# Optimization experiments

Measured on AMD Instinct MI355X. Metric: run time of the kernel, lower is better.

## Reference

```python
import jax, jax.numpy as jnp
import numpy as np

D_MODEL = 1024
NUM_HEADS = 16
MAX_SEQ_LEN = 2048
THETA = 10000.0
D_K = D_MODEL // NUM_HEADS


def setup_inputs() -> dict:
    key = jax.random.key(0)
    ks = jax.random.split(key, 5)
    x = jax.random.normal(ks[0], (2, 2048, D_MODEL), dtype=jnp.float32)
    token_positions = jnp.arange(2048, dtype=jnp.int32)
    s = 1.0 / np.sqrt(D_MODEL)
    w_q = jax.random.normal(ks[1], (D_MODEL, D_MODEL), dtype=jnp.float32) * s
    w_k = jax.random.normal(ks[2], (D_MODEL, D_MODEL), dtype=jnp.float32) * s
    w_v = jax.random.normal(ks[3], (D_MODEL, D_MODEL), dtype=jnp.float32) * s
    w_o = jax.random.normal(ks[4], (D_MODEL, D_MODEL), dtype=jnp.float32) * s
    return {"x": x, "token_positions": token_positions,
            "w_q": w_q, "w_k": w_k, "w_v": w_v, "w_o": w_o}


def _rope_tables():
    inv_freq = 1.0 / (THETA ** (jnp.arange(0, D_K, 2, dtype=jnp.float32) / D_K))
    angles = jnp.arange(MAX_SEQ_LEN, dtype=jnp.float32)[:, None] * inv_freq[None, :]
    return jnp.cos(angles), jnp.sin(angles)  # [max_seq_len, d_k//2]


def _apply_rope(x, cos, sin):
    # x: [..., s, d_k]; interleaved-pair rotation, cos/sin: [s, d_k//2]
    x0 = x[..., 0::2]
    x1 = x[..., 1::2]
    y0 = x0 * cos - x1 * sin
    y1 = x0 * sin + x1 * cos
    return jnp.stack((y0, y1), axis=-1).reshape(x.shape)


def reference(x, token_positions, w_q, w_k, w_v, w_o):
    b, s, _ = x.shape
    h, dk = NUM_HEADS, D_K
    # torch Linear: y = x @ W^T
    q = (x @ w_q.T).reshape(b, s, h, dk).transpose(0, 2, 1, 3)  # [b,h,s,dk]
    k = (x @ w_k.T).reshape(b, s, h, dk).transpose(0, 2, 1, 3)
    v = (x @ w_v.T).reshape(b, s, h, dk).transpose(0, 2, 1, 3)
    cos_c, sin_c = _rope_tables()
    cos = cos_c[token_positions]  # [s, dk//2]
    sin = sin_c[token_positions]
    q = _apply_rope(q, cos, sin)
    k = _apply_rope(k, cos, sin)
    scores = jnp.einsum('bhqd,bhkd->bhqk', q, k) / jnp.sqrt(jnp.float32(dk))
    causal = jnp.tril(jnp.ones((s, s), dtype=bool))
    scores = jnp.where(causal, scores, -jnp.inf)
    attn = jax.nn.softmax(scores, axis=-1)
    out = jnp.einsum('bhqk,bhkd->bhqd', attn, v)
    out = out.transpose(0, 2, 1, 3).reshape(b, s, h * dk)
    return out @ w_o.T
```

## Files before the change

kernel.cpp:

```cpp
#include <hip/hip_runtime.h>
#include <cstdint>
#include <cstddef>

#define DEV static __device__ __forceinline__

typedef __attribute__((ext_vector_type(8))) short bf16x8;
typedef __attribute__((ext_vector_type(4))) float f32x4;

DEV uint16_t f2bf(float f) {
  uint32_t u = __builtin_bit_cast(uint32_t, f);
  u += 0x7FFFu + ((u >> 16) & 1u);
  return (uint16_t)(u >> 16);
}

DEV uint32_t packbf(float a, float b) {
  return (__builtin_bit_cast(uint32_t, a) >> 16) |
         (__builtin_bit_cast(uint32_t, b) & 0xFFFF0000u);
}

DEV float fexp2(float x) { return __builtin_amdgcn_exp2f(x); }

template <int CTRL>
DEV float dppf(float v) {
  return __builtin_bit_cast(
      float, __builtin_amdgcn_update_dpp(0, __builtin_bit_cast(int, v), CTRL, 0xF, 0xF, true));
}

DEV float swz16(float v) {
  return __builtin_bit_cast(
      float, __builtin_amdgcn_ds_swizzle(__builtin_bit_cast(int, v), 0x401F));
}
DEV float bperm(int lane_idx, float v) {
  return __builtin_bit_cast(
      float, __builtin_amdgcn_ds_bpermute(lane_idx << 2, __builtin_bit_cast(int, v)));
}

DEV void load_lds16(const void* g, void* l) {
  auto gp = reinterpret_cast<const uint32_t __attribute__((address_space(1)))*>(
      reinterpret_cast<uintptr_t>(g));
  auto lp = reinterpret_cast<uint32_t __attribute__((address_space(3)))*>(
      reinterpret_cast<uintptr_t>(l));
  __builtin_amdgcn_global_load_lds(gp, lp, 16, 0, 0);
}

__global__ __launch_bounds__(256) void cvt_all(const float* __restrict__ x,
                                               const float* __restrict__ wq,
                                               const float* __restrict__ wk,
                                               const float* __restrict__ wv,
                                               const float* __restrict__ wo,
                                               const int* __restrict__ tokpos,
                                               uint16_t* __restrict__ dst,
                                               float2* __restrict__ rtab) {
  int bx = blockIdx.x;
  if (bx >= 8192) {
    int idx = (bx - 8192) * 256 + threadIdx.x;
    int s = idx >> 5, f = idx & 31;
    float invf = __expf(-0.28782314f * (float)f);
    float pos = (float)tokpos[s];
    float sn, cs;
    __sincosf(pos * invf, &sn, &cs);
    rtab[idx] = make_float2(cs, sn);
    return;
  }
  int gi = bx * 1024 + threadIdx.x * 4;
  const float* s;
  int li;
  if (gi < 4194304) {
    s = x; li = gi;
  } else {
    int j = gi - 4194304;
    int r = j >> 20;
    li = j & 1048575;
    s = (r == 0) ? wq : (r == 1) ? wk : (r == 2) ? wv : wo;
  }
  float4 v = *reinterpret_cast<const float4*>(s + li);
  ushort4 o;
  o.x = f2bf(v.x); o.y = f2bf(v.y); o.z = f2bf(v.z); o.w = f2bf(v.w);
  *reinterpret_cast<ushort4*>(dst + gi) = o;
}

__global__ __launch_bounds__(512) void gemm_qkv(const uint16_t* __restrict__ A,
                                                const uint16_t* __restrict__ Wqkv,
                                                uint16_t* __restrict__ QK,
                                                uint16_t* __restrict__ VTb,
                                                const float2* __restrict__ rtab) {
  __shared__ union {
    struct { uint16_t a[2][128 * 64]; uint16_t b[2][128 * 64]; } st;
    uint16_t t[128 * 128];
  } sm;

  const int tid = threadIdx.x;
  const int lane = tid & 63, w = tid >> 6;
  const int q = lane >> 4, l16 = lane & 15;
  const int wm = w >> 1, wn = w & 1;

  const int orig = blockIdx.y * 24 + blockIdx.x;
  const int logical = (orig & 7) * 96 + (orig >> 3);
  const int bm = logical / 24, bn = logical % 24;
  const int wsel = bn >> 3;

  const f32x4 z4 = {0.f, 0.f, 0.f, 0.f};
  f32x4 acc[2][4];
#pragma unroll
  for (int i = 0; i < 2; ++i)
#pragma unroll
    for (int j = 0; j < 4; ++j) acc[i][j] = z4;

  const int srow = tid >> 3, sslot = tid & 7;
  const uint16_t* Ab = A + (size_t)bm * 128 * 1024;
  const uint16_t* Bb = Wqkv + (size_t)bn * 128 * 1024;

  auto stage = [&](int buf, int k0) {
#pragma unroll
    for (int is = 0; is < 2; ++is) {
      int row = is * 64 + srow;
      int gch = sslot ^ (row & 7);
      char* la = (char*)sm.st.a[buf] + (is * 64 + w * 8) * 128;
      char* lb = (char*)sm.st.b[buf] + (is * 64 + w * 8) * 128;
      load_lds16(Ab + (size_t)row * 1024 + k0 + gch * 8, la);
      load_lds16(Bb + (size_t)row * 1024 + k0 + gch * 8, lb);
    }
  };

  stage(0, 0);
  for (int t = 0; t < 16; ++t) {
    const int cur = t & 1;
    __syncthreads();
    if (t + 1 < 16) stage(cur ^ 1, (t + 1) * 64);
#pragma unroll
    for (int ks = 0; ks < 2; ++ks) {
      bf16x8 af[2], bfr[4];
#pragma unroll
      for (int i = 0; i < 2; ++i) {
        int ra = wm * 32 + i * 16 + l16;
        af[i] = *reinterpret_cast<const bf16x8*>(sm.st.a[cur] + ra * 64 +
                                                 (((ks * 4 + q) ^ (ra & 7)) * 8));
      }
#pragma unroll
      for (int j = 0; j < 4; ++j) {
        int rb = wn * 64 + j * 16 + l16;
        bfr[j] = *reinterpret_cast<const bf16x8*>(sm.st.b[cur] + rb * 64 +
                                                  (((ks * 4 + q) ^ (rb & 7)) * 8));
      }
#pragma unroll
      for (int i = 0; i < 2; ++i)
#pragma unroll
        for (int j = 0; j < 4; ++j)
          acc[i][j] =
              __builtin_amdgcn_mfma_f32_16x16x32_bf16(af[i], bfr[j], acc[i][j], 0, 0, 0);
    }
  }

  if (wsel < 2) {
    uint16_t* O = QK + (size_t)wsel * 4194304;
    const float scq = (wsel == 0) ? 0.18033688f : 1.0f;
#pragma unroll
    for (int j = 0; j < 4; ++j) {
      int gn = bn * 128 + wn * 64 + j * 16 + l16;
      int cn = gn & 1023;
      int f = (gn & 63) >> 1;
      float sgn = (lane & 1) ? 1.f : -1.f;
#pragma unroll
      for (int i = 0; i < 2; ++i) {
#pragma unroll
        for (int r = 0; r < 4; ++r) {
          int gm = bm * 128 + wm * 32 + i * 16 + q * 4 + r;
          float2 cssn = rtab[(gm & 2047) * 32 + f];
          float v = acc[i][j][r];
          float o = dppf<0xB1>(v);
          O[(size_t)gm * 1024 + cn] = f2bf((v * cssn.x + sgn * o * cssn.y) * scq);
        }
      }
    }
  } else {
    const int bnv = bn & 7;
    __syncthreads();
#pragma unroll
    for (int i = 0; i < 2; ++i)
#pragma unroll
      for (int j = 0; j < 4; ++j)
#pragma unroll
        for (int r = 0; r < 4; ++r) {
          int mL = wm * 32 + i * 16 + q * 4 + r;
          int nL = wn * 64 + j * 16 + l16;
          int ch = (mL >> 3) ^ (nL & 15);
          sm.t[nL * 128 + ch * 8 + (mL & 7)] = f2bf(acc[i][j][r]);
        }
    __syncthreads();
    const int b = (bm * 128) >> 11;
    const int sblk = (bm * 128) & 2047;
#pragma unroll
    for (int it = 0; it < 4; ++it) {
      int nL = it * 32 + (tid >> 4);
      int mch = tid & 15;
      int slot = mch ^ (nL & 15);
      bf16x8 vv = *reinterpret_cast<const bf16x8*>(sm.t + nL * 128 + slot * 8);
      int gn = bnv * 128 + nL;
      int h = gn >> 6, d = gn & 63;
      *reinterpret_cast<bf16x8*>(VTb + ((size_t)((b * 16 + h) * 64 + d)) * 2048 + sblk +
                                 mch * 8) = vv;
    }
  }
}

__global__ __launch_bounds__(512) void gemm_out(const uint16_t* __restrict__ A,
                                                const uint16_t* __restrict__ Bw,
                                                float* __restrict__ O) {
  __shared__ uint16_t sa[2][128 * 64];
  __shared__ uint16_t sb[2][64 * 64];

  const int tid = threadIdx.x;
  const int lane = tid & 63, w = tid >> 6;
  const int q = lane >> 4, l16 = lane & 15;
  const int wm = w >> 1, wn = w & 1;

  const int orig = blockIdx.y * 16 + blockIdx.x;
  const int logical = (orig & 7) * 64 + (orig >> 3);
  const int bm = logical / 16, bn = logical % 16;

  const f32x4 z4 = {0.f, 0.f, 0.f, 0.f};
  f32x4 acc[2][2];
#pragma unroll
  for (int i = 0; i < 2; ++i)
#pragma unroll
    for (int j = 0; j < 2; ++j) acc[i][j] = z4;

  const int srow = tid >> 3, sslot = tid & 7;
  const uint16_t* Ab = A + (size_t)bm * 128 * 1024;
  const uint16_t* Bb = Bw + (size_t)bn * 64 * 1024;

  auto stage = [&](int buf, int k0) {
#pragma unroll
    for (int is = 0; is < 2; ++is) {
      int row = is * 64 + srow;
      int gch = sslot ^ (row & 7);
      load_lds16(Ab + (size_t)row * 1024 + k0 + gch * 8,
                 (char*)sa[buf] + (is * 64 + w * 8) * 128);
    }
    {
      int row = srow;
      int gch = sslot ^ (row & 7);
      load_lds16(Bb + (size_t)row * 1024 + k0 + gch * 8,
                 (char*)sb[buf] + (w * 8) * 128);
    }
  };

  stage(0, 0);
  for (int t = 0; t < 16; ++t) {
    const int cur = t & 1;
    __syncthreads();
    if (t + 1 < 16) stage(cur ^ 1, (t + 1) * 64);
#pragma unroll
    for (int ks = 0; ks < 2; ++ks) {
      bf16x8 af[2], bfr[2];
#pragma unroll
      for (int i = 0; i < 2; ++i) {
        int ra = wm * 32 + i * 16 + l16;
        af[i] = *reinterpret_cast<const bf16x8*>(sa[cur] + ra * 64 +
                                                 (((ks * 4 + q) ^ (ra & 7)) * 8));
      }
#pragma unroll
      for (int j = 0; j < 2; ++j) {
        int rb = wn * 32 + j * 16 + l16;
        bfr[j] = *reinterpret_cast<const bf16x8*>(sb[cur] + rb * 64 +
                                                  (((ks * 4 + q) ^ (rb & 7)) * 8));
      }
#pragma unroll
      for (int i = 0; i < 2; ++i)
#pragma unroll
        for (int j = 0; j < 2; ++j)
          acc[i][j] =
              __builtin_amdgcn_mfma_f32_16x16x32_bf16(af[i], bfr[j], acc[i][j], 0, 0, 0);
    }
  }

#pragma unroll
  for (int i = 0; i < 2; ++i)
#pragma unroll
    for (int r = 0; r < 4; ++r) {
      int gm = bm * 128 + wm * 32 + i * 16 + q * 4 + r;
#pragma unroll
      for (int j = 0; j < 2; ++j) {
        int gn = bn * 64 + wn * 32 + j * 16 + l16;
        O[(size_t)gm * 1024 + gn] = acc[i][j][r];
      }
    }
}

__global__ __launch_bounds__(512) void flash_attn(const uint16_t* __restrict__ Q,
                                                  const uint16_t* __restrict__ K,
                                                  const uint16_t* __restrict__ VT,
                                                  uint16_t* __restrict__ AO) {
  __shared__ uint16_t ksm[2][128 * 64];
  __shared__ uint16_t vsm[64 * 128];
  __shared__ uint16_t psm[8][16 * 128];

  const int tid = threadIdx.x;
  const int lane = tid & 63, w = tid >> 6;
  const int q = lane >> 4, l16 = lane & 15;

  const int orig = blockIdx.y * 8 + blockIdx.x;
  const int logical = (orig & 7) * 32 + (orig >> 3);
  const int p = logical & 7;
  const int bh = logical >> 3;
  const int b = bh >> 4, h = bh & 15;

  const size_t baseBS = (size_t)b * 2048 * 1024 + h * 64;
  const size_t baseVT = (size_t)bh * 64 * 2048;
  uint16_t* pw = psm[w];
  const f32x4 z4 = {0.f, 0.f, 0.f, 0.f};

  auto stageK = [&](int buf, int kt) {
#pragma unroll
    for (int is = 0; is < 2; ++is) {
      int row = is * 64 + (tid >> 3);
      int gch = (tid & 7) ^ (row & 7);
      load_lds16(K + baseBS + (size_t)(kt * 128 + row) * 1024 + gch * 8,
                 (char*)ksm[buf] + (is * 64 + w * 8) * 128);
    }
  };
  auto stageV = [&](int kt) {
#pragma unroll
    for (int is = 0; is < 2; ++is) {
      int row = is * 32 + (tid >> 4);
      int gch = (tid & 15) ^ (row & 15);
      load_lds16(VT + baseVT + (size_t)row * 2048 + kt * 128 + gch * 8,
                 (char*)vsm + (is * 32 + w * 4) * 256);
    }
  };

  for (int t = 0; t < 2; ++t) {
    const int qt = t ? (15 - p) : p;
    const int r0 = qt * 128 + w * 16;
    const int nkt = qt + 1;

    bf16x8 qf[2];
#pragma unroll
    for (int ks = 0; ks < 2; ++ks)
      qf[ks] = *reinterpret_cast<const bf16x8*>(
          Q + baseBS + (size_t)(r0 + l16) * 1024 + ks * 32 + q * 8);

    f32x4 oa[4];
#pragma unroll
    for (int di = 0; di < 4; ++di) oa[di] = z4;
    float m2 = -1e30f, li = 0.f;

    __syncthreads();
    stageK(0, 0);

    for (int kt = 0; kt < nkt; ++kt) {
      const int cur = kt & 1;
      __syncthreads();
      stageV(kt);

      f32x4 sc[8];
#pragma unroll
      for (int nj = 0; nj < 8; ++nj) sc[nj] = z4;
#pragma unroll
      for (int ks = 0; ks < 2; ++ks) {
        bf16x8 kf[8];
#pragma unroll
        for (int nj = 0; nj < 8; ++nj) {
          int rk = nj * 16 + l16;
          kf[nj] = *reinterpret_cast<const bf16x8*>(ksm[cur] + rk * 64 +
                                                    (((ks * 4 + q) ^ (rk & 7)) * 8));
        }
        __builtin_amdgcn_s_setprio(1);
#pragma unroll
        for (int nj = 0; nj < 8; ++nj)
          sc[nj] =
              __builtin_amdgcn_mfma_f32_16x16x32_bf16(kf[nj], qf[ks], sc[nj], 0, 0, 0);
        __builtin_amdgcn_s_setprio(0);
      }

      if (kt == nkt - 1) {
#pragma unroll
        for (int nj = 0; nj < 8; ++nj)
#pragma unroll
          for (int r = 0; r < 4; ++r) {
            int col = nj * 16 + q * 4 + r;
            int row = w * 16 + l16;
            if (col > row) sc[nj][r] = -1e30f;
          }
      }

      f32x4 m4 = sc[0];
#pragma unroll
      for (int nj = 1; nj < 8; ++nj) {
#pragma unroll
        for (int r = 0; r < 4; ++r) m4[r] = fmaxf(m4[r], sc[nj][r]);
      }
      float pmax = fmaxf(fmaxf(m4[0], m4[1]), fmaxf(m4[2], m4[3]));
      pmax = fmaxf(pmax, swz16(pmax));
      pmax = fmaxf(pmax, bperm(lane ^ 32, pmax));

      if (__any(pmax > m2 + 8.f)) {
        float mn = fmaxf(m2, pmax);
        float al = fexp2(m2 - mn);
        m2 = mn;
        li *= al;
        float ar[4];
#pragma unroll
        for (int r = 0; r < 4; ++r)
          ar[r] = bperm((lane & 48) | (q * 4 + r), al);
#pragma unroll
        for (int di = 0; di < 4; ++di)
#pragma unroll
          for (int r = 0; r < 4; ++r) oa[di][r] *= ar[r];
      }

      {
        uint16_t* pwr = pw + l16 * 128 + (q & 1) * 4;
        const int swz = l16 & 15;
#pragma unroll
        for (int nj = 0; nj < 8; ++nj) {
          float e0 = fexp2(sc[nj][0] - m2);
          float e1 = fexp2(sc[nj][1] - m2);
          float e2 = fexp2(sc[nj][2] - m2);
          float e3 = fexp2(sc[nj][3] - m2);
          li += (e0 + e1) + (e2 + e3);
          uint64_t pk = (uint64_t)packbf(e0, e1) | ((uint64_t)packbf(e2, e3) << 32);
          *reinterpret_cast<uint64_t*>(
              pwr + (((nj * 2 + (q >> 1)) ^ swz) * 8)) = pk;
        }
      }

      __syncthreads();

      if (kt + 1 < nkt) stageK(cur ^ 1, kt + 1);

#pragma unroll
      for (int ks = 0; ks < 4; ++ks) {
        bf16x8 pf = *reinterpret_cast<const bf16x8*>(pw + l16 * 128 +
                                                     (((ks * 4 + q) ^ (l16 & 15)) * 8));
        bf16x8 vf[4];
#pragma unroll
        for (int di = 0; di < 4; ++di) {
          int vr = di * 16 + l16;
          vf[di] = *reinterpret_cast<const bf16x8*>(vsm + vr * 128 +
                                                    (((ks * 4 + q) ^ (vr & 15)) * 8));
        }
        __builtin_amdgcn_s_setprio(1);
#pragma unroll
        for (int di = 0; di < 4; ++di)
          oa[di] =
              __builtin_amdgcn_mfma_f32_16x16x32_bf16(pf, vf[di], oa[di], 0, 0, 0);
        __builtin_amdgcn_s_setprio(0);
      }
    }

    float lf = li;
    lf += swz16(lf);
    lf += bperm(lane ^ 32, lf);
    float invL = 1.f / lf;
    float inv_r[4];
#pragma unroll
    for (int r = 0; r < 4; ++r)
      inv_r[r] = bperm((lane & 48) | (q * 4 + r), invL);
#pragma unroll
    for (int r = 0; r < 4; ++r) {
      int gm = r0 + q * 4 + r;
#pragma unroll
      for (int di = 0; di < 4; ++di)
        AO[baseBS + (size_t)gm * 1024 + di * 16 + l16] = f2bf(oa[di][r] * inv_r[r]);
    }
  }
}

extern "C" void kernel_launch(void* const* d_in, const int* in_sizes, int n_in,
                              void* d_out, int out_size, void* d_ws, size_t ws_size,
                              hipStream_t stream) {
  (void)in_sizes; (void)n_in; (void)out_size; (void)ws_size;
  const float* x = (const float*)d_in[0];
  const int* tokpos = (const int*)d_in[1];
  const float* wq = (const float*)d_in[2];
  const float* wk = (const float*)d_in[3];
  const float* wv = (const float*)d_in[4];
  const float* wo = (const float*)d_in[5];
  float* out = (float*)d_out;

  uint16_t* ws = (uint16_t*)d_ws;
  uint16_t* xb = ws;
  uint16_t* wqb = xb + 4194304;
  uint16_t* wob = wqb + 3145728;
  uint16_t* Qb = wob + 1048576;
  uint16_t* VTb = Qb + 8388608;
  uint16_t* AOb = VTb + 4194304;
  float2* rtab = (float2*)AOb;

  cvt_all<<<8448, 256, 0, stream>>>(x, wq, wk, wv, wo, tokpos, xb, rtab);

  gemm_qkv<<<dim3(24, 32), 512, 0, stream>>>(xb, wqb, Qb, VTb, rtab);

  flash_attn<<<dim3(8, 32), 512, 0, stream>>>(Qb, Qb + 4194304, VTb, AOb);

  gemm_out<<<dim3(16, 32), 512, 0, stream>>>(AOb, wob, out);
}
```

Baseline: 164.5 us.

## Process both paired query tiles concurrently in one 1024-thread attention block

The attention kernel now launches 1024 threads per block, split into two 8-wave groups that handle the early and late query tiles of a causal pair at the same time. The groups share each staged K/V tile, so K/V for the shared prefix is loaded once instead of twice. The short-tile group idles once its causal range ends. K double buffering is dropped to make room for the larger P scratch in LDS. This trades fewer K/V loads and barrier rounds for wasted waves on the short tile, a less overlapped K load, and higher register pressure at 1024 threads.

```diff
diff --git a/kernel.cpp b/kernel.cpp
--- a/kernel.cpp
+++ b/kernel.cpp
@@ -287,16 +287,17 @@
     }
 }
 
-__global__ __launch_bounds__(512) void flash_attn(const uint16_t* __restrict__ Q,
-                                                  const uint16_t* __restrict__ K,
-                                                  const uint16_t* __restrict__ VT,
-                                                  uint16_t* __restrict__ AO) {
-  __shared__ uint16_t ksm[2][128 * 64];
+__global__ __launch_bounds__(1024) void flash_attn(const uint16_t* __restrict__ Q,
+                                                   const uint16_t* __restrict__ K,
+                                                   const uint16_t* __restrict__ VT,
+                                                   uint16_t* __restrict__ AO) {
+  __shared__ uint16_t ksm[128 * 64];
   __shared__ uint16_t vsm[64 * 128];
-  __shared__ uint16_t psm[8][16 * 128];
+  __shared__ uint16_t psm[16][16 * 128];
 
   const int tid = threadIdx.x;
   const int lane = tid & 63, w = tid >> 6;
+  const int g = w >> 3, wl = w & 7;
   const int q = lane >> 4, l16 = lane & 15;
 
   const int orig = blockIdx.y * 8 + blockIdx.x;
@@ -310,50 +311,44 @@
   uint16_t* pw = psm[w];
   const f32x4 z4 = {0.f, 0.f, 0.f, 0.f};
 
-  auto stageK = [&](int buf, int kt) {
-#pragma unroll
-    for (int is = 0; is < 2; ++is) {
-      int row = is * 64 + (tid >> 3);
-      int gch = (tid & 7) ^ (row & 7);
-      load_lds16(K + baseBS + (size_t)(kt * 128 + row) * 1024 + gch * 8,
-                 (char*)ksm[buf] + (is * 64 + w * 8) * 128);
-    }
+  const int qt = g ? (15 - p) : p;
+  const int r0 = qt * 128 + wl * 16;
+  const int nkt = 16 - p;
+
+  auto stageK = [&](int kt) {
+    int row = tid >> 3;
+    int gch = (tid & 7) ^ (row & 7);
+    load_lds16(K + baseBS + (size_t)(kt * 128 + row) * 1024 + gch * 8,
+               (char*)ksm + w * 1024);
   };
   auto stageV = [&](int kt) {
-#pragma unroll
-    for (int is = 0; is < 2; ++is) {
-      int row = is * 32 + (tid >> 4);
-      int gch = (tid & 15) ^ (row & 15);
-      load_lds16(VT + baseVT + (size_t)row * 2048 + kt * 128 + gch * 8,
-                 (char*)vsm + (is * 32 + w * 4) * 256);
-    }
+    int row = tid >> 4;
+    int gch = (tid & 15) ^ (row & 15);
+    load_lds16(VT + baseVT + (size_t)row * 2048 + kt * 128 + gch * 8,
+               (char*)vsm + w * 1024);
   };
 
-  for (int t = 0; t < 2; ++t) {
-    const int qt = t ? (15 - p) : p;
-    const int r0 = qt * 128 + w * 16;
-    const int nkt = qt + 1;
-
-    bf16x8 qf[2];
-#pragma unroll
-    for (int ks = 0; ks < 2; ++ks)
-      qf[ks] = *reinterpret_cast<const bf16x8*>(
-          Q + baseBS + (size_t)(r0 + l16) * 1024 + ks * 32 + q * 8);
-
-    f32x4 oa[4];
-#pragma unroll
-    for (int di = 0; di < 4; ++di) oa[di] = z4;
-    float m2 = -1e30f, li = 0.f;
-
-    __syncthreads();
-    stageK(0, 0);
-
-    for (int kt = 0; kt < nkt; ++kt) {
-      const int cur = kt & 1;
-      __syncthreads();
-      stageV(kt);
-
-      f32x4 sc[8];
+  bf16x8 qf[2];
+#pragma unroll
+  for (int ks = 0; ks < 2; ++ks)
+    qf[ks] = *reinterpret_cast<const bf16x8*>(
+        Q + baseBS + (size_t)(r0 + l16) * 1024 + ks * 32 + q * 8);
+
+  f32x4 oa[4];
+#pragma unroll
+  for (int di = 0; di < 4; ++di) oa[di] = z4;
+  float m2 = -1e30f, li = 0.f;
+
+  stageK(0);
+
+  for (int kt = 0; kt < nkt; ++kt) {
+    __syncthreads();
+    stageV(kt);
+
+    const bool act = (kt <= qt);
+
+    f32x4 sc[8];
+    if (act) {
 #pragma unroll
       for (int nj = 0; nj < 8; ++nj) sc[nj] = z4;
 #pragma unroll
@@ -362,7 +357,7 @@
 #pragma unroll
         for (int nj = 0; nj < 8; ++nj) {
           int rk = nj * 16 + l16;
-          kf[nj] = *reinterpret_cast<const bf16x8*>(ksm[cur] + rk * 64 +
+          kf[nj] = *reinterpret_cast<const bf16x8*>(ksm + rk * 64 +
                                                     (((ks * 4 + q) ^ (rk & 7)) * 8));
         }
         __builtin_amdgcn_s_setprio(1);
@@ -373,13 +368,13 @@
         __builtin_amdgcn_s_setprio(0);
       }
 
-      if (kt == nkt - 1) {
+      if (kt == qt) {
 #pragma unroll
         for (int nj = 0; nj < 8; ++nj)
 #pragma unroll
           for (int r = 0; r < 4; ++r) {
             int col = nj * 16 + q * 4 + r;
-            int row = w * 16 + l16;
+            int row = wl * 16 + l16;
             if (col > row) sc[nj][r] = -1e30f;
           }
       }
@@ -424,11 +419,13 @@
               pwr + (((nj * 2 + (q >> 1)) ^ swz) * 8)) = pk;
         }
       }
-
-      __syncthreads();
-
-      if (kt + 1 < nkt) stageK(cur ^ 1, kt + 1);
-
+    }
+
+    __syncthreads();
+
+    if (kt + 1 < nkt) stageK(kt + 1);
+
+    if (act) {
 #pragma unroll
       for (int ks = 0; ks < 4; ++ks) {
         bf16x8 pf = *reinterpret_cast<const bf16x8*>(pw + l16 * 128 +
@@ -448,22 +445,22 @@
         __builtin_amdgcn_s_setprio(0);
       }
     }
-
-    float lf = li;
-    lf += swz16(lf);
-    lf += bperm(lane ^ 32, lf);
-    float invL = 1.f / lf;
-    float inv_r[4];
-#pragma unroll
-    for (int r = 0; r < 4; ++r)
-      inv_r[r] = bperm((lane & 48) | (q * 4 + r), invL);
-#pragma unroll
-    for (int r = 0; r < 4; ++r) {
-      int gm = r0 + q * 4 + r;
-#pragma unroll
-      for (int di = 0; di < 4; ++di)
-        AO[baseBS + (size_t)gm * 1024 + di * 16 + l16] = f2bf(oa[di][r] * inv_r[r]);
-    }
+  }
+
+  float lf = li;
+  lf += swz16(lf);
+  lf += bperm(lane ^ 32, lf);
+  float invL = 1.f / lf;
+  float inv_r[4];
+#pragma unroll
+  for (int r = 0; r < 4; ++r)
+    inv_r[r] = bperm((lane & 48) | (q * 4 + r), invL);
+#pragma unroll
+  for (int r = 0; r < 4; ++r) {
+    int gm = r0 + q * 4 + r;
+#pragma unroll
+    for (int di = 0; di < 4; ++di)
+      AO[baseBS + (size_t)gm * 1024 + di * 16 + l16] = f2bf(oa[di][r] * inv_r[r]);
   }
 }
 
@@ -492,7 +489,7 @@
 
   gemm_qkv<<<dim3(24, 32), 512, 0, stream>>>(xb, wqb, Qb, VTb, rtab);
 
-  flash_attn<<<dim3(8, 32), 512, 0, stream>>>(Qb, Qb + 4194304, VTb, AOb);
+  flash_attn<<<dim3(8, 32), 1024, 0, stream>>>(Qb, Qb + 4194304, VTb, AOb);
 
   gemm_out<<<dim3(16, 32), 512, 0, stream>>>(AOb, wob, out);
 }
```

Result: no change. 165.5 us (+0.6%).
